# Kernel optimization log

Measured on AMD Instinct MI355X. Metric: run time of the kernel, lower is better.

## Reference

```python
import jax, jax.numpy as jnp
import numpy as np

N, S, R, CM = 1, 128, 256, 256
C, CZ = 32, 128


def setup_inputs() -> dict:
    key = jax.random.key(0)
    k1, k2, k3, k4 = jax.random.split(key, 4)
    return {
        "msa_repr": jax.random.normal(k1, (N, S, R, CM), dtype=jnp.float32),
        "left_proj": jax.random.normal(k2, (CM, C), dtype=jnp.float32) * 0.05,
        "right_proj": jax.random.normal(k3, (CM, C), dtype=jnp.float32) * 0.05,
        "out_proj": jax.random.normal(k4, (C * C, CZ), dtype=jnp.float32) * 0.05,
    }


def reference(msa_repr, left_proj, right_proj, out_proj):
    # msa_repr: [N, S, R, CM]
    # Project to left/right activations and move R before S
    # (equivalent to torch matmul + transpose(-2, -3)).
    a = jnp.einsum("nsrm,mc->nrsc", msa_repr, left_proj)   # [N, R, S, C]
    b = jnp.einsum("nsrm,mc->nrsc", msa_repr, right_proj)  # [N, R, S, C]
    # Outer product contracted over the MSA dim S:
    # outer[n, r, t, c, e] = sum_s a[n, r, s, c] * b[n, t, s, e]
    outer = jnp.einsum("nrsc,ntse->nrtce", a, b)            # [N, R, R, C, C]
    n, r, t = outer.shape[:3]
    outer = outer.reshape(n, r, t, C * C)                   # [N, R, R, C*C]
    # Output projection to pair channels cz
    return outer @ out_proj                                 # [N, R, R, CZ]
```

## Files before the change

### kernel.cpp

```cpp
#include <hip/hip_runtime.h>

typedef __bf16 bf16x8 __attribute__((ext_vector_type(8)));
typedef __bf16 bf16x4 __attribute__((ext_vector_type(4)));
typedef float f32x16 __attribute__((ext_vector_type(16)));
typedef float f32x4 __attribute__((ext_vector_type(4)));

constexpr int S = 128, R = 256, CM = 256, C = 32, CZ = 128;

#define MFMA __builtin_amdgcn_mfma_f32_32x32x16_bf16

__device__ __forceinline__ bf16x4 cvt4(float a, float b, float c, float d) {
    bf16x4 r;
    r[0] = (__bf16)a; r[1] = (__bf16)b; r[2] = (__bf16)c; r[3] = (__bf16)d;
    return r;
}

__global__ __launch_bounds__(256) void k_prep(const float* __restrict__ W,
                                              const float* __restrict__ Lp,
                                              const float* __restrict__ Rp,
                                              __bf16* __restrict__ WTf,
                                              __bf16* __restrict__ WLRT) {
    int b = blockIdx.x;
    if (b < 512) {
        int g = b * 256 + threadIdx.x;
        int cz = g & 127;
        int k = g >> 7;
        int e = k >> 5, c = k & 31;
        float v = W[(size_t)(c * 32 + e) * 128 + cz];
        WTf[((size_t)(k >> 3) * 128 + cz) * 8 + (k & 7)] = (__bf16)v;
    } else {
        int c = b - 512;
        int m = threadIdx.x;
        const float* src = (c < 32) ? Lp : Rp;
        WLRT[(size_t)c * 256 + m] = (__bf16)src[(size_t)m * 32 + (c & 31)];
    }
}

__global__ __launch_bounds__(256) void k_proj(const float* __restrict__ msa,
                                              const __bf16* __restrict__ WLRT,
                                              __bf16* __restrict__ aTf,
                                              __bf16* __restrict__ bTf) {
    __shared__ __align__(16) __bf16 As[32 * 256];
    __shared__ __align__(16) char Pp[2 * 4096];
    const int r = blockIdx.x;
    const int sq = blockIdx.y;
    const int t = threadIdx.x;

#pragma unroll
    for (int it = 0; it < 8; ++it) {
        int idx = it * 256 + t;
        int row = idx >> 6;
        int cg = idx & 63;
        float4 v = *(const float4*)&msa[((size_t)(sq * 32 + row) * R + r) * CM + cg * 4];
        bf16x4 h = cvt4(v.x, v.y, v.z, v.w);
        int P = (cg >> 1) ^ (row & 15);
        *(bf16x4*)((char*)As + row * 512 + P * 16 + (cg & 1) * 8) = h;
    }
    __syncthreads();

    const int w = t >> 6;
    const int l = t & 63;
    const int l31 = t & 31;
    const int kh = (t >> 5) & 1;
    const int sd = w & 1;
    const int ksh = w >> 1;

    f32x16 acc;
#pragma unroll
    for (int q = 0; q < 16; ++q) acc[q] = 0.f;

    const bf16x8* wb = (const bf16x8*)&WLRT[(size_t)(sd * 32 + l31) * 256 + 8 * kh];
    const char* arow = (const char*)As + l31 * 512;

    __builtin_amdgcn_s_setprio(1);
#pragma unroll
    for (int j = 0; j < 8; ++j) {
        int ks = ksh * 8 + j;
        int P = (2 * ks + kh) ^ (l31 & 15);
        bf16x8 af = *(const bf16x8*)(arow + P * 16);
        acc = MFMA(af, wb[2 * ks], acc, 0, 0, 0);
    }
    __builtin_amdgcn_s_setprio(0);

    char* pbase = Pp + (size_t)sd * 4096;
    if (ksh == 1) {
#pragma unroll
        for (int pc = 0; pc < 4; ++pc) {
            f32x4 v;
            v[0] = acc[4 * pc + 0]; v[1] = acc[4 * pc + 1];
            v[2] = acc[4 * pc + 2]; v[3] = acc[4 * pc + 3];
            *(f32x4*)(pbase + ((pc * 64) + l) * 16) = v;
        }
    }
    __syncthreads();
    if (ksh == 0) {
#pragma unroll
        for (int pc = 0; pc < 4; ++pc) {
            f32x4 v = *(const f32x4*)(pbase + ((pc * 64) + l) * 16);
            acc[4 * pc + 0] += v[0]; acc[4 * pc + 1] += v[1];
            acc[4 * pc + 2] += v[2]; acc[4 * pc + 3] += v[3];
        }
        __bf16* dst = sd ? bTf : aTf;
#pragma unroll
        for (int q = 0; q < 4; ++q) {
            size_t base = (size_t)r * 4096 + (size_t)(2 * sq + (q >> 1)) * 512 +
                          (size_t)(q & 1) * 256 + (size_t)l31 * 8 + 4 * kh;
            *(bf16x4*)&dst[base] = cvt4(acc[4 * q + 0], acc[4 * q + 1],
                                        acc[4 * q + 2], acc[4 * q + 3]);
        }
    }
}

__global__ __launch_bounds__(512, 2) void k_main(const __bf16* __restrict__ aTf,
                                                 const __bf16* __restrict__ bTf,
                                                 const __bf16* __restrict__ WTf,
                                                 float* __restrict__ out) {
    __shared__ __align__(16) __bf16 Gs[64 * 1024];

    const int t = threadIdx.x;
    const int w = t >> 6;
    const int l = t & 63;
    const int lane = l & 31;
    const int kh = l >> 5;
    const int r0 = blockIdx.x * 8;
    const int t0 = blockIdx.y * 8;

    const int rg = w & 3;
    const int tg = w >> 2;

    f32x16 acc[2][4];
#pragma unroll
    for (int i = 0; i < 2; ++i)
#pragma unroll
        for (int j = 0; j < 4; ++j)
#pragma unroll
            for (int q = 0; q < 16; ++q) acc[i][j][q] = 0.f;

    const bf16x8* ap0 = (const bf16x8*)aTf + ((size_t)(r0 + 2 * rg + 0) * 512 + kh * 32 + lane);
    const bf16x8* ap1 = (const bf16x8*)aTf + ((size_t)(r0 + 2 * rg + 1) * 512 + kh * 32 + lane);
    const bf16x8* bp0 = (const bf16x8*)bTf + ((size_t)(t0 + 4 * tg + 0) * 512 + kh * 32 + lane);
    const bf16x8* bp1 = (const bf16x8*)bTf + ((size_t)(t0 + 4 * tg + 1) * 512 + kh * 32 + lane);
    const bf16x8* bp2 = (const bf16x8*)bTf + ((size_t)(t0 + 4 * tg + 2) * 512 + kh * 32 + lane);
    const bf16x8* bp3 = (const bf16x8*)bTf + ((size_t)(t0 + 4 * tg + 3) * 512 + kh * 32 + lane);

    bf16x8 Ap[4][2], Bp[4][4];
#pragma unroll
    for (int s = 0; s < 4; ++s) {
        Ap[s][0] = ap0[s * 64]; Ap[s][1] = ap1[s * 64];
        Bp[s][0] = bp0[s * 64]; Bp[s][1] = bp1[s * 64];
        Bp[s][2] = bp2[s * 64]; Bp[s][3] = bp3[s * 64];
    }
    __builtin_amdgcn_sched_barrier(0);

#pragma unroll
    for (int ks = 0; ks < 8; ++ks) {
        const int s = ks & 3;
        __builtin_amdgcn_s_setprio(1);
        acc[0][0] = MFMA(Ap[s][0], Bp[s][0], acc[0][0], 0, 0, 0);
        acc[0][1] = MFMA(Ap[s][0], Bp[s][1], acc[0][1], 0, 0, 0);
        acc[0][2] = MFMA(Ap[s][0], Bp[s][2], acc[0][2], 0, 0, 0);
        acc[0][3] = MFMA(Ap[s][0], Bp[s][3], acc[0][3], 0, 0, 0);
        acc[1][0] = MFMA(Ap[s][1], Bp[s][0], acc[1][0], 0, 0, 0);
        acc[1][1] = MFMA(Ap[s][1], Bp[s][1], acc[1][1], 0, 0, 0);
        acc[1][2] = MFMA(Ap[s][1], Bp[s][2], acc[1][2], 0, 0, 0);
        acc[1][3] = MFMA(Ap[s][1], Bp[s][3], acc[1][3], 0, 0, 0);
        __builtin_amdgcn_s_setprio(0);
        if (ks + 4 < 8) {
            const int kn = ks + 4;
            Ap[s][0] = ap0[kn * 64]; Ap[s][1] = ap1[kn * 64];
            Bp[s][0] = bp0[kn * 64]; Bp[s][1] = bp1[kn * 64];
            Bp[s][2] = bp2[kn * 64]; Bp[s][3] = bp3[kn * 64];
        }
    }

#pragma unroll
    for (int i = 0; i < 2; ++i) {
#pragma unroll
        for (int j = 0; j < 4; ++j) {
            int p = (2 * rg + i) * 8 + 4 * tg + j;
            unsigned prow = (unsigned)p * 2048;
#pragma unroll
            for (int q = 0; q < 4; ++q) {
                int Lc = lane * 4 + q;
                int P = Lc ^ (p & 15) ^ (lane & 7);
                *(bf16x4*)((char*)Gs + prow + (unsigned)P * 16 + kh * 8) =
                    cvt4(acc[i][j][4 * q + 0], acc[i][j][4 * q + 1],
                         acc[i][j][4 * q + 2], acc[i][j][4 * q + 3]);
            }
        }
    }
    __syncthreads();

    const int kq = w >> 1;
    const int ng = w & 1;
    const int czl0 = ng * 64 + lane;
    const int czl1 = czl0 + 32;
    const bf16x8* wb0 = (const bf16x8*)WTf + ((size_t)kh * 128 + czl0);
    const bf16x8* wb1 = (const bf16x8*)WTf + ((size_t)kh * 128 + czl1);
    const unsigned prow0 = (unsigned)lane * 2048;
    const unsigned prow1 = (unsigned)(lane + 32) * 2048;
    const int p15 = lane & 15;

    f32x16 o00, o01, o10, o11;
#pragma unroll
    for (int q = 0; q < 16; ++q) { o00[q] = 0.f; o01[q] = 0.f; o10[q] = 0.f; o11[q] = 0.f; }

    bf16x8 Wp[16][2];
#pragma unroll
    for (int s = 0; s < 16; ++s) {
        const int kk = kq * 16 + s;
        Wp[s][0] = wb0[(size_t)kk * 256];
        Wp[s][1] = wb1[(size_t)kk * 256];
    }
    __builtin_amdgcn_sched_barrier(0);

    bf16x8 Gp[2][2];
#define LDG(sl, kk) do { \
    int Lr = (kk) * 2 + kh; \
    int P = Lr ^ p15 ^ ((Lr >> 2) & 7); \
    Gp[sl][0] = *(const bf16x8*)((const char*)Gs + prow0 + (unsigned)P * 16); \
    Gp[sl][1] = *(const bf16x8*)((const char*)Gs + prow1 + (unsigned)P * 16); } while (0)

    LDG(0, kq * 16 + 0);
    LDG(1, kq * 16 + 1);
#pragma unroll
    for (int j = 0; j < 16; ++j) {
        const int s = j & 1;
        __builtin_amdgcn_s_setprio(1);
        o00 = MFMA(Gp[s][0], Wp[j][0], o00, 0, 0, 0);
        o01 = MFMA(Gp[s][0], Wp[j][1], o01, 0, 0, 0);
        o10 = MFMA(Gp[s][1], Wp[j][0], o10, 0, 0, 0);
        o11 = MFMA(Gp[s][1], Wp[j][1], o11, 0, 0, 0);
        __builtin_amdgcn_s_setprio(0);
        if (j + 2 < 16) LDG(s, kq * 16 + j + 2);
    }
    __syncthreads();

    {
        char* pr = (char*)Gs + (size_t)w * 16384;
        const f32x16* os[4] = {&o00, &o01, &o10, &o11};
#pragma unroll
        for (int s2 = 0; s2 < 4; ++s2) {
#pragma unroll
            for (int pc = 0; pc < 4; ++pc) {
                f32x4 v;
                v[0] = (*os[s2])[4 * pc + 0]; v[1] = (*os[s2])[4 * pc + 1];
                v[2] = (*os[s2])[4 * pc + 2]; v[3] = (*os[s2])[4 * pc + 3];
                *(f32x4*)(pr + ((s2 * 4 + pc) * 64 + l) * 16) = v;
            }
        }
    }
    __syncthreads();

    {
        const int ngx = w >> 2;
        const int mix = (w >> 1) & 1;
        const int nix = w & 1;
        const int s2 = mix * 2 + nix;
        f32x16 sm;
#pragma unroll
        for (int q = 0; q < 16; ++q) sm[q] = 0.f;
#pragma unroll
        for (int kq2 = 0; kq2 < 4; ++kq2) {
            const char* pr = (const char*)Gs + (size_t)(kq2 * 2 + ngx) * 16384;
#pragma unroll
            for (int pc = 0; pc < 4; ++pc) {
                f32x4 v = *(const f32x4*)(pr + ((s2 * 4 + pc) * 64 + l) * 16);
                sm[4 * pc + 0] += v[0]; sm[4 * pc + 1] += v[1];
                sm[4 * pc + 2] += v[2]; sm[4 * pc + 3] += v[3];
            }
        }
        const int czl = ngx * 64 + nix * 32 + (l & 31);
        const int khx = l >> 5;
#pragma unroll
        for (int reg = 0; reg < 16; ++reg) {
            int pl = mix * 32 + (reg & 3) + 8 * (reg >> 2) + 4 * khx;
            int prr = pl >> 3, ptt = pl & 7;
            out[((size_t)(r0 + prr) * 256 + (t0 + ptt)) * 128 + czl] = sm[reg];
        }
    }
}

extern "C" void kernel_launch(void* const* d_in, const int* in_sizes, int n_in,
                              void* d_out, int out_size, void* d_ws, size_t ws_size,
                              hipStream_t stream) {
    const float* msa = (const float*)d_in[0];
    const float* left = (const float*)d_in[1];
    const float* right = (const float*)d_in[2];
    const float* W = (const float*)d_in[3];

    __bf16* aTf = (__bf16*)d_ws;
    __bf16* bTf = aTf + (size_t)R * 4096;
    __bf16* WTf = bTf + (size_t)R * 4096;
    __bf16* WLRT = WTf + (size_t)128 * 1024;
    float* outp = (float*)d_out;

    k_prep<<<576, 256, 0, stream>>>(W, left, right, WTf, WLRT);
    k_proj<<<dim3(256, 4), 256, 0, stream>>>(msa, WLRT, aTf, bTf);
    k_main<<<dim3(32, 32), 512, 0, stream>>>(aTf, bTf, WTf, outp);
}
```

Baseline: 60.83 us.

## Loop k_main over t-tiles with double-buffered LDS and register-resident projection weights

k_main now processes 32 t columns per block in 8 iterations, and the grid shrinks from 32x32 to 32x8 blocks. The a fragments and a per-wave half of the output projection weights stay in registers across iterations. The next b tile is prefetched with inline global loads while the current outer product runs, and the outer-product stage of one tile overlaps the projection stage of the previous tile through two LDS buffers. The K reduction is split across only two wave halves, so less partial-sum traffic goes through LDS. In exchange, register pressure and LDS use rise, occupancy drops to one block per CU, and fewer blocks are launched.

```diff
diff --git a/kernel.cpp b/kernel.cpp
--- a/kernel.cpp
+++ b/kernel.cpp
@@ -41,7 +41,7 @@
                                               __bf16* __restrict__ aTf,
                                               __bf16* __restrict__ bTf) {
     __shared__ __align__(16) __bf16 As[32 * 256];
-    __shared__ __align__(16) char Pp[2 * 4096];
+    __shared__ __align__(16) char Pq[2 * 4096];
     const int r = blockIdx.x;
     const int sq = blockIdx.y;
     const int t = threadIdx.x;
@@ -82,7 +82,7 @@
     }
     __builtin_amdgcn_s_setprio(0);
 
-    char* pbase = Pp + (size_t)sd * 4096;
+    char* pbase = Pq + (size_t)sd * 4096;
     if (ksh == 1) {
 #pragma unroll
         for (int pc = 0; pc < 4; ++pc) {
@@ -111,11 +111,12 @@
     }
 }
 
-__global__ __launch_bounds__(512, 2) void k_main(const __bf16* __restrict__ aTf,
+__global__ __launch_bounds__(512, 1) void k_main(const __bf16* __restrict__ aTf,
                                                  const __bf16* __restrict__ bTf,
                                                  const __bf16* __restrict__ WTf,
                                                  float* __restrict__ out) {
-    __shared__ __align__(16) __bf16 Gs[64 * 1024];
+    __shared__ __align__(16) __bf16 Gs[2 * 32768];
+    __shared__ __align__(16) float Pp[4096];
 
     const int t = threadIdx.x;
     const int w = t >> 6;
@@ -123,160 +124,150 @@
     const int lane = l & 31;
     const int kh = l >> 5;
     const int r0 = blockIdx.x * 8;
-    const int t0 = blockIdx.y * 8;
+    const int tbase = blockIdx.y * 32;
 
     const int rg = w & 3;
     const int tg = w >> 2;
-
-    f32x16 acc[2][4];
-#pragma unroll
-    for (int i = 0; i < 2; ++i)
-#pragma unroll
-        for (int j = 0; j < 4; ++j)
-#pragma unroll
-            for (int q = 0; q < 16; ++q) acc[i][j][q] = 0.f;
-
-    const bf16x8* ap0 = (const bf16x8*)aTf + ((size_t)(r0 + 2 * rg + 0) * 512 + kh * 32 + lane);
-    const bf16x8* ap1 = (const bf16x8*)aTf + ((size_t)(r0 + 2 * rg + 1) * 512 + kh * 32 + lane);
-    const bf16x8* bp0 = (const bf16x8*)bTf + ((size_t)(t0 + 4 * tg + 0) * 512 + kh * 32 + lane);
-    const bf16x8* bp1 = (const bf16x8*)bTf + ((size_t)(t0 + 4 * tg + 1) * 512 + kh * 32 + lane);
-    const bf16x8* bp2 = (const bf16x8*)bTf + ((size_t)(t0 + 4 * tg + 2) * 512 + kh * 32 + lane);
-    const bf16x8* bp3 = (const bf16x8*)bTf + ((size_t)(t0 + 4 * tg + 3) * 512 + kh * 32 + lane);
-
-    bf16x8 Ap[4][2], Bp[4][4];
-#pragma unroll
-    for (int s = 0; s < 4; ++s) {
-        Ap[s][0] = ap0[s * 64]; Ap[s][1] = ap1[s * 64];
-        Bp[s][0] = bp0[s * 64]; Bp[s][1] = bp1[s * 64];
-        Bp[s][2] = bp2[s * 64]; Bp[s][3] = bp3[s * 64];
-    }
-    __builtin_amdgcn_sched_barrier(0);
-
-#pragma unroll
-    for (int ks = 0; ks < 8; ++ks) {
-        const int s = ks & 3;
-        __builtin_amdgcn_s_setprio(1);
-        acc[0][0] = MFMA(Ap[s][0], Bp[s][0], acc[0][0], 0, 0, 0);
-        acc[0][1] = MFMA(Ap[s][0], Bp[s][1], acc[0][1], 0, 0, 0);
-        acc[0][2] = MFMA(Ap[s][0], Bp[s][2], acc[0][2], 0, 0, 0);
-        acc[0][3] = MFMA(Ap[s][0], Bp[s][3], acc[0][3], 0, 0, 0);
-        acc[1][0] = MFMA(Ap[s][1], Bp[s][0], acc[1][0], 0, 0, 0);
-        acc[1][1] = MFMA(Ap[s][1], Bp[s][1], acc[1][1], 0, 0, 0);
-        acc[1][2] = MFMA(Ap[s][1], Bp[s][2], acc[1][2], 0, 0, 0);
-        acc[1][3] = MFMA(Ap[s][1], Bp[s][3], acc[1][3], 0, 0, 0);
-        __builtin_amdgcn_s_setprio(0);
-        if (ks + 4 < 8) {
-            const int kn = ks + 4;
-            Ap[s][0] = ap0[kn * 64]; Ap[s][1] = ap1[kn * 64];
-            Bp[s][0] = bp0[kn * 64]; Bp[s][1] = bp1[kn * 64];
-            Bp[s][2] = bp2[kn * 64]; Bp[s][3] = bp3[kn * 64];
-        }
-    }
-
-#pragma unroll
-    for (int i = 0; i < 2; ++i) {
-#pragma unroll
-        for (int j = 0; j < 4; ++j) {
-            int p = (2 * rg + i) * 8 + 4 * tg + j;
-            unsigned prow = (unsigned)p * 2048;
-#pragma unroll
-            for (int q = 0; q < 4; ++q) {
-                int Lc = lane * 4 + q;
-                int P = Lc ^ (p & 15) ^ (lane & 7);
-                *(bf16x4*)((char*)Gs + prow + (unsigned)P * 16 + kh * 8) =
-                    cvt4(acc[i][j][4 * q + 0], acc[i][j][4 * q + 1],
-                         acc[i][j][4 * q + 2], acc[i][j][4 * q + 3]);
-            }
-        }
-    }
-    __syncthreads();
-
-    const int kq = w >> 1;
-    const int ng = w & 1;
-    const int czl0 = ng * 64 + lane;
-    const int czl1 = czl0 + 32;
-    const bf16x8* wb0 = (const bf16x8*)WTf + ((size_t)kh * 128 + czl0);
-    const bf16x8* wb1 = (const bf16x8*)WTf + ((size_t)kh * 128 + czl1);
-    const unsigned prow0 = (unsigned)lane * 2048;
-    const unsigned prow1 = (unsigned)(lane + 32) * 2048;
-    const int p15 = lane & 15;
-
-    f32x16 o00, o01, o10, o11;
-#pragma unroll
-    for (int q = 0; q < 16; ++q) { o00[q] = 0.f; o01[q] = 0.f; o10[q] = 0.f; o11[q] = 0.f; }
-
-    bf16x8 Wp[16][2];
-#pragma unroll
-    for (int s = 0; s < 16; ++s) {
-        const int kk = kq * 16 + s;
-        Wp[s][0] = wb0[(size_t)kk * 256];
-        Wp[s][1] = wb1[(size_t)kk * 256];
-    }
-    __builtin_amdgcn_sched_barrier(0);
-
-    bf16x8 Gp[2][2];
-#define LDG(sl, kk) do { \
-    int Lr = (kk) * 2 + kh; \
-    int P = Lr ^ p15 ^ ((Lr >> 2) & 7); \
-    Gp[sl][0] = *(const bf16x8*)((const char*)Gs + prow0 + (unsigned)P * 16); \
-    Gp[sl][1] = *(const bf16x8*)((const char*)Gs + prow1 + (unsigned)P * 16); } while (0)
-
-    LDG(0, kq * 16 + 0);
-    LDG(1, kq * 16 + 1);
-#pragma unroll
-    for (int j = 0; j < 16; ++j) {
-        const int s = j & 1;
-        __builtin_amdgcn_s_setprio(1);
-        o00 = MFMA(Gp[s][0], Wp[j][0], o00, 0, 0, 0);
-        o01 = MFMA(Gp[s][0], Wp[j][1], o01, 0, 0, 0);
-        o10 = MFMA(Gp[s][1], Wp[j][0], o10, 0, 0, 0);
-        o11 = MFMA(Gp[s][1], Wp[j][1], o11, 0, 0, 0);
-        __builtin_amdgcn_s_setprio(0);
-        if (j + 2 < 16) LDG(s, kq * 16 + j + 2);
-    }
-    __syncthreads();
-
+    const int ng = w & 3;
+    const int mh = w >> 2;
+
+    bf16x8 Aa[2][8];
     {
-        char* pr = (char*)Gs + (size_t)w * 16384;
-        const f32x16* os[4] = {&o00, &o01, &o10, &o11};
-#pragma unroll
-        for (int s2 = 0; s2 < 4; ++s2) {
-#pragma unroll
-            for (int pc = 0; pc < 4; ++pc) {
-                f32x4 v;
-                v[0] = (*os[s2])[4 * pc + 0]; v[1] = (*os[s2])[4 * pc + 1];
-                v[2] = (*os[s2])[4 * pc + 2]; v[3] = (*os[s2])[4 * pc + 3];
-                *(f32x4*)(pr + ((s2 * 4 + pc) * 64 + l) * 16) = v;
-            }
-        }
-    }
-    __syncthreads();
-
+        const bf16x8* ap0 = (const bf16x8*)aTf + ((size_t)(r0 + 2 * rg + 0) * 512 + kh * 32 + lane);
+        const bf16x8* ap1 = (const bf16x8*)aTf + ((size_t)(r0 + 2 * rg + 1) * 512 + kh * 32 + lane);
+#pragma unroll
+        for (int ks = 0; ks < 8; ++ks) { Aa[0][ks] = ap0[ks * 64]; Aa[1][ks] = ap1[ks * 64]; }
+    }
+    const int czl = ng * 32 + lane;
+    bf16x8 Wp[32];
     {
-        const int ngx = w >> 2;
-        const int mix = (w >> 1) & 1;
-        const int nix = w & 1;
-        const int s2 = mix * 2 + nix;
-        f32x16 sm;
-#pragma unroll
-        for (int q = 0; q < 16; ++q) sm[q] = 0.f;
-#pragma unroll
-        for (int kq2 = 0; kq2 < 4; ++kq2) {
-            const char* pr = (const char*)Gs + (size_t)(kq2 * 2 + ngx) * 16384;
-#pragma unroll
-            for (int pc = 0; pc < 4; ++pc) {
-                f32x4 v = *(const f32x4*)(pr + ((s2 * 4 + pc) * 64 + l) * 16);
-                sm[4 * pc + 0] += v[0]; sm[4 * pc + 1] += v[1];
-                sm[4 * pc + 2] += v[2]; sm[4 * pc + 3] += v[3];
-            }
-        }
-        const int czl = ngx * 64 + nix * 32 + (l & 31);
-        const int khx = l >> 5;
-#pragma unroll
-        for (int reg = 0; reg < 16; ++reg) {
-            int pl = mix * 32 + (reg & 3) + 8 * (reg >> 2) + 4 * khx;
-            int prr = pl >> 3, ptt = pl & 7;
-            out[((size_t)(r0 + prr) * 256 + (t0 + ptt)) * 128 + czl] = sm[reg];
+        const bf16x8* wptr = (const bf16x8*)WTf + ((size_t)mh * 8192 + (size_t)kh * 128 + czl);
+#pragma unroll
+        for (int s = 0; s < 32; ++s) Wp[s] = wptr[(size_t)s * 256];
+    }
+    bf16x8 Bc[2][8];
+    {
+        const bf16x8* bq0 = (const bf16x8*)bTf + ((size_t)(tbase + 2 * tg + 0) * 512 + kh * 32 + lane);
+        const bf16x8* bq1 = (const bf16x8*)bTf + ((size_t)(tbase + 2 * tg + 1) * 512 + kh * 32 + lane);
+#pragma unroll
+        for (int ks = 0; ks < 8; ++ks) { Bc[0][ks] = bq0[ks * 64]; Bc[1][ks] = bq1[ks * 64]; }
+    }
+
+    const unsigned prowG = (unsigned)lane * 2048;
+    const int p15r = lane & 15;
+
+#pragma unroll 1
+    for (int i = 0; i <= 8; ++i) {
+        char* gw = (char*)Gs + (size_t)(i & 1) * 65536;
+        const char* gr = (const char*)Gs + (size_t)((i ^ 1) & 1) * 65536;
+
+        if (i < 8) {
+            asm volatile("s_waitcnt vmcnt(0)");
+            __builtin_amdgcn_sched_barrier(0);
+
+            f32x16 acc[2][2];
+#pragma unroll
+            for (int ii = 0; ii < 2; ++ii)
+#pragma unroll
+                for (int jj = 0; jj < 2; ++jj)
+#pragma unroll
+                    for (int q = 0; q < 16; ++q) acc[ii][jj][q] = 0.f;
+
+            const char* bn0 = (const char*)bTf +
+                ((size_t)(tbase + 4 * (i + 1) + 2 * tg + 0) * 512 + kh * 32 + lane) * 16;
+            const char* bn1 = (const char*)bTf +
+                ((size_t)(tbase + 4 * (i + 1) + 2 * tg + 1) * 512 + kh * 32 + lane) * 16;
+
+#pragma unroll
+            for (int ks = 0; ks < 8; ++ks) {
+                __builtin_amdgcn_s_setprio(1);
+                acc[0][0] = MFMA(Aa[0][ks], Bc[0][ks], acc[0][0], 0, 0, 0);
+                acc[0][1] = MFMA(Aa[0][ks], Bc[1][ks], acc[0][1], 0, 0, 0);
+                acc[1][0] = MFMA(Aa[1][ks], Bc[0][ks], acc[1][0], 0, 0, 0);
+                acc[1][1] = MFMA(Aa[1][ks], Bc[1][ks], acc[1][1], 0, 0, 0);
+                __builtin_amdgcn_s_setprio(0);
+                if (i + 1 < 8) {
+                    asm volatile("global_load_dwordx4 %0, %1, off"
+                                 : "=v"(Bc[0][ks]) : "v"(bn0 + (size_t)ks * 1024));
+                    asm volatile("global_load_dwordx4 %0, %1, off"
+                                 : "=v"(Bc[1][ks]) : "v"(bn1 + (size_t)ks * 1024));
+                }
+            }
+
+#pragma unroll
+            for (int ii = 0; ii < 2; ++ii) {
+#pragma unroll
+                for (int jj = 0; jj < 2; ++jj) {
+                    int p = (2 * rg + ii) * 4 + 2 * tg + jj;
+                    unsigned prow = (unsigned)p * 2048;
+#pragma unroll
+                    for (int q = 0; q < 4; ++q) {
+                        int Lc = lane * 4 + q;
+                        int P = Lc ^ (p & 15) ^ (lane & 7);
+                        *(bf16x4*)(gw + prow + (unsigned)P * 16 + kh * 8) =
+                            cvt4(acc[ii][jj][4 * q + 0], acc[ii][jj][4 * q + 1],
+                                 acc[ii][jj][4 * q + 2], acc[ii][jj][4 * q + 3]);
+                    }
+                }
+            }
+        }
+
+        f32x16 oA, oB;
+        if (i >= 1) {
+#pragma unroll
+            for (int q = 0; q < 16; ++q) { oA[q] = 0.f; oB[q] = 0.f; }
+
+            bf16x8 Gp[4];
+            const int kb = mh * 32;
+#define LDG1(sl, ss) do { \
+    int Lr = (kb + (ss)) * 2 + kh; \
+    int P = Lr ^ p15r ^ ((Lr >> 2) & 7); \
+    Gp[sl] = *(const bf16x8*)(gr + prowG + (unsigned)P * 16); } while (0)
+
+            LDG1(0, 0); LDG1(1, 1); LDG1(2, 2); LDG1(3, 3);
+#pragma unroll
+            for (int s = 0; s < 32; ++s) {
+                __builtin_amdgcn_s_setprio(1);
+                if (s & 1) oB = MFMA(Gp[s & 3], Wp[s], oB, 0, 0, 0);
+                else       oA = MFMA(Gp[s & 3], Wp[s], oA, 0, 0, 0);
+                __builtin_amdgcn_s_setprio(0);
+                if (s + 4 < 32) LDG1(s & 3, s + 4);
+            }
+        }
+
+        asm volatile("s_waitcnt lgkmcnt(0)");
+        __builtin_amdgcn_s_barrier();
+
+        if (i >= 1) {
+            f32x16 osum = oA + oB;
+            if (mh == 1) {
+                char* pb = (char*)Pp + (size_t)ng * 4096;
+#pragma unroll
+                for (int pc = 0; pc < 4; ++pc) {
+                    f32x4 v;
+                    v[0] = osum[4 * pc + 0]; v[1] = osum[4 * pc + 1];
+                    v[2] = osum[4 * pc + 2]; v[3] = osum[4 * pc + 3];
+                    *(f32x4*)(pb + (pc * 64 + l) * 16) = v;
+                }
+            }
+            asm volatile("s_waitcnt lgkmcnt(0)");
+            __builtin_amdgcn_s_barrier();
+            if (mh == 0) {
+                const char* pb = (const char*)Pp + (size_t)ng * 4096;
+#pragma unroll
+                for (int pc = 0; pc < 4; ++pc) {
+                    f32x4 v = *(const f32x4*)(pb + (pc * 64 + l) * 16);
+                    osum[4 * pc + 0] += v[0]; osum[4 * pc + 1] += v[1];
+                    osum[4 * pc + 2] += v[2]; osum[4 * pc + 3] += v[3];
+                }
+                const int tb2 = tbase + 4 * (i - 1);
+#pragma unroll
+                for (int reg = 0; reg < 16; ++reg) {
+                    int pl = (reg & 3) + 8 * (reg >> 2) + 4 * kh;
+                    int rl = pl >> 2, tl = pl & 3;
+                    out[((size_t)(r0 + rl) * 256 + (tb2 + tl)) * 128 + czl] = osum[reg];
+                }
+            }
         }
     }
 }
@@ -297,5 +288,5 @@
 
     k_prep<<<576, 256, 0, stream>>>(W, left, right, WTf, WLRT);
     k_proj<<<dim3(256, 4), 256, 0, stream>>>(msa, WLRT, aTf, bTf);
-    k_main<<<dim3(32, 32), 512, 0, stream>>>(aTf, bTf, WTf, outp);
-}
+    k_main<<<dim3(32, 8), 512, 0, stream>>>(aTf, bTf, WTf, outp);
+}
```

Measured after the change: 204.9 us. +236.8%, slower.
